# Kernel tuning notes

Hardware: AMD Instinct MI355X
Metric: run time of the kernel (lower is better)

The kernel has to match this reference:

```python
import jax, jax.numpy as jnp
import numpy as np
from jax import lax

PART = 224   # PART_IMAGE_SIZE
PAD = 224    # PAD_SIZE
TOPN = 4
IOU_THRESH = 0.25
N_ANCHORS = 1614


def _conv(x, w, b, stride, pad):
    y = lax.conv_general_dilated(x, w, (stride, stride), [(pad, pad), (pad, pad)],
                                 dimension_numbers=('NCHW', 'OIHW', 'NCHW'))
    return y + b[None, :, None, None]


def _iou(box, boxes):
    # box [4], boxes [N,4] as (y0,x0,y1,x1)
    yy0 = jnp.maximum(box[0], boxes[:, 0]); xx0 = jnp.maximum(box[1], boxes[:, 1])
    yy1 = jnp.minimum(box[2], boxes[:, 2]); xx1 = jnp.minimum(box[3], boxes[:, 3])
    inter = jnp.clip(yy1 - yy0, 0.0) * jnp.clip(xx1 - xx0, 0.0)
    a = (box[2] - box[0]) * (box[3] - box[1])
    areas = (boxes[:, 2] - boxes[:, 0]) * (boxes[:, 3] - boxes[:, 1])
    return inter / (a + areas - inter)


def _nms(scores, boxes):
    # hard NMS keeping TOPN boxes; returns indices [TOPN]
    valid = jnp.ones(scores.shape, dtype=bool)
    idxs = []
    for _ in range(TOPN):
        i = jnp.argmax(jnp.where(valid, scores, -jnp.inf))
        idxs.append(i)
        valid = valid & (_iou(boxes[i], boxes) <= IOU_THRESH)
    return jnp.stack(idxs)


def _crop_resize(img, box):
    # img [3,Hp,Wp] padded image, box [4] float; bilinear, align_corners=True,
    # matching F.interpolate(x_pad[:, :, y0:y1, x0:x1], (PART, PART))
    Hp, Wp = img.shape[1], img.shape[2]
    def coords(c0, c1, L):
        t = jnp.arange(PART, dtype=img.dtype) / (PART - 1)
        c = c0 + (c1 - 1.0 - c0) * t          # absolute source coordinate
        cf = jnp.floor(c)
        lo = jnp.clip(cf.astype(jnp.int32), 0, L - 1)
        hi = jnp.clip(lo + 1, 0, L - 1)
        return lo, hi, c - cf
    yl, yh, wy = coords(box[0], box[2], Hp)
    xl, xh, wx = coords(box[1], box[3], Wp)
    g = lambda yi, xi: img[:, yi[:, None], xi[None, :]]   # [3,PART,PART]
    return ((1 - wy)[:, None] * ((1 - wx) * g(yl, xl) + wx * g(yl, xh))
            + wy[:, None] * ((1 - wx) * g(yh, xl) + wx * g(yh, xh)))


def setup_inputs() -> dict:
    key = jax.random.key(0)
    ks = jax.random.split(key, 20)
    x = jax.random.uniform(ks[0], (16, 3, 448, 448), dtype=jnp.float32)
    rpn_feature = jax.random.normal(ks[1], (16, 2048, 14, 14), dtype=jnp.float32)
    # valid boxes inside the padded 896x896 image
    y0 = jax.random.randint(ks[2], (N_ANCHORS,), 0, 560)
    x0 = jax.random.randint(ks[3], (N_ANCHORS,), 0, 560)
    h = jax.random.randint(ks[4], (N_ANCHORS,), 32, 336)
    w = jax.random.randint(ks[5], (N_ANCHORS,), 32, 336)
    anchors = jnp.stack([y0, x0, jnp.minimum(y0 + h, 896), jnp.minimum(x0 + w, 896)], axis=1).astype(jnp.int32)
    s = 0.02
    inp = {
        'x': x, 'rpn_feature': rpn_feature, 'anchors': anchors,
        'w_down1': jax.random.normal(ks[6], (128, 2048, 3, 3), jnp.float32) * s,
        'b_down1': jnp.zeros((128,), jnp.float32),
        'w_down2': jax.random.normal(ks[7], (128, 128, 3, 3), jnp.float32) * s,
        'b_down2': jnp.zeros((128,), jnp.float32),
        'w_down3': jax.random.normal(ks[8], (128, 128, 3, 3), jnp.float32) * s,
        'b_down3': jnp.zeros((128,), jnp.float32),
        'w_tidy1': jax.random.normal(ks[9], (6, 128, 1, 1), jnp.float32) * s,
        'b_tidy1': jnp.zeros((6,), jnp.float32),
        'w_tidy2': jax.random.normal(ks[10], (6, 128, 1, 1), jnp.float32) * s,
        'b_tidy2': jnp.zeros((6,), jnp.float32),
        'w_tidy3': jax.random.normal(ks[11], (9, 128, 1, 1), jnp.float32) * s,
        'b_tidy3': jnp.zeros((9,), jnp.float32),
    }
    return inp


def reference(x, rpn_feature, anchors,
              w_down1, b_down1, w_down2, b_down2, w_down3, b_down3,
              w_tidy1, b_tidy1, w_tidy2, b_tidy2, w_tidy3, b_tidy3):
    B = x.shape[0]
    # ProposalNet
    d1 = jax.nn.relu(_conv(rpn_feature, w_down1, b_down1, 1, 1))   # [B,128,14,14]
    d2 = jax.nn.relu(_conv(d1, w_down2, b_down2, 2, 1))            # [B,128,7,7]
    d3 = jax.nn.relu(_conv(d2, w_down3, b_down3, 2, 1))            # [B,128,4,4]
    t1 = _conv(d1, w_tidy1, b_tidy1, 1, 0).reshape(B, -1)
    t2 = _conv(d2, w_tidy2, b_tidy2, 1, 0).reshape(B, -1)
    t3 = _conv(d3, w_tidy3, b_tidy3, 1, 0).reshape(B, -1)
    rpn_score = jnp.concatenate([t1, t2, t3], axis=1)              # [B, 1614]
    boxes = anchors.astype(x.dtype)                                # [N,4]
    top_n_index = jax.vmap(lambda s: _nms(s, boxes))(rpn_score)    # [B,TOPN]
    top_n_prob = jnp.take_along_axis(rpn_score, top_n_index, axis=1)
    x_pad = jnp.pad(x, ((0, 0), (0, 0), (PAD, PAD), (PAD, PAD)))   # [B,3,896,896]
    sel_boxes = boxes[top_n_index]                                 # [B,TOPN,4]
    part_imgs = jax.vmap(lambda img, bxs: jax.vmap(lambda b: _crop_resize(img, b))(bxs))(x_pad, sel_boxes)
    # part_imgs: [B,TOPN,3,PART,PART]
    return rpn_score, top_n_index, top_n_prob, part_imgs
```

## Files before the change

### kernel.cpp

```cpp
#include <hip/hip_runtime.h>
#include <hip/hip_bf16.h>

#define NB 16
#define NA 1614
#define NBP (NB * 196 * 128)

typedef __bf16 bf16x8 __attribute__((ext_vector_type(8)));
typedef float f32x4 __attribute__((ext_vector_type(4)));

__device__ __forceinline__ unsigned short f2bf(float v) {
  unsigned u = __float_as_uint(v);
  unsigned r = (u + 0x7FFFu + ((u >> 16) & 1u)) >> 16;
  return (unsigned short)r;
}
__device__ __forceinline__ float bf2f(unsigned short s) {
  return __uint_as_float(((unsigned)s) << 16);
}

__global__ __launch_bounds__(256)
void prep(const float* __restrict__ w, const float* __restrict__ in,
          unsigned short* __restrict__ wTh, unsigned short* __restrict__ wTl,
          unsigned short* __restrict__ aTh, unsigned short* __restrict__ aTl) {
  __shared__ float s[32 * 201];
  const int bid = blockIdx.x;
  if (bid < 1024) {
    const int chunk = bid & 63, b = bid >> 6;
    const float* src = in + ((size_t)b * 2048 + chunk * 32) * 196;
#pragma unroll
    for (int r = 0; r < 7; r++) {
      int e = threadIdx.x + 256 * r;
      if (e < 1568) {
        int ic = e / 49, f = e - ic * 49;
        float4 v = ((const float4*)(src + (size_t)ic * 196))[f];
        float* d = s + ic * 201 + f * 4;
        d[0] = v.x; d[1] = v.y; d[2] = v.z; d[3] = v.w;
      }
    }
    __syncthreads();
    unsigned short* oh = aTh + (size_t)bid * (196 * 32);
    unsigned short* ol = aTl + (size_t)bid * (196 * 32);
#pragma unroll
    for (int r = 0; r < 4; r++) {
      int e = threadIdx.x + 256 * r;
      if (e < 784) {
        int pos = e >> 2, part = e & 3;
        unsigned short hv[8], lv[8];
#pragma unroll
        for (int j = 0; j < 8; j++) {
          float v = s[(part * 8 + j) * 201 + pos];
          unsigned short h = f2bf(v);
          hv[j] = h;
          lv[j] = f2bf(v - bf2f(h));
        }
        ((uint4*)oh)[e] = *(uint4*)hv;
        ((uint4*)ol)[e] = *(uint4*)lv;
      }
    }
  } else {
    int e = (bid - 1024) * 256 + threadIdx.x;
    if (e < 9 * 128 * 2048) {
      int tap = e / (128 * 2048);
      int rem = e - tap * (128 * 2048);
      int oc = rem >> 11, ic = rem & 2047;
      int kcp = ic >> 7, ks = (ic >> 5) & 3, icq = (ic >> 3) & 3, j = ic & 7;
      size_t g2 = ((size_t)(kcp * 36 + tap * 4 + ks) << 12) + oc * 32 + icq * 8 + j;
      float v = w[((size_t)oc * 2048 + ic) * 9 + tap];
      unsigned short h = f2bf(v);
      wTh[g2] = h;
      wTl[g2] = f2bf(v - bf2f(h));
    }
  }
}

#define APL 2192
#define ABUF (4 * APL)

#define LOADB(H, L, T, K)                                                     \
  {                                                                           \
    const size_t o_ = ((size_t)(kc * 36 + (T) * 4 + (K)) << 12) + bln;        \
    const unsigned short* ph_ = wTh + o_;                                     \
    const unsigned short* pq_ = wTl + o_;                                     \
    H[0] = *(const bf16x8*)(ph_);                                             \
    H[1] = *(const bf16x8*)(ph_ + 512);                                       \
    H[2] = *(const bf16x8*)(ph_ + 1024);                                      \
    H[3] = *(const bf16x8*)(ph_ + 1536);                                      \
    L[0] = *(const bf16x8*)(pq_);                                             \
    L[1] = *(const bf16x8*)(pq_ + 512);                                       \
    L[2] = *(const bf16x8*)(pq_ + 1024);                                      \
    L[3] = *(const bf16x8*)(pq_ + 1536);                                      \
  }

#define STEP(IT, BUH, BUL, BNH, BNL)                                          \
  {                                                                           \
    const int it_ = (IT);                                                     \
    const int ks_ = it_ / 9, tap_ = it_ - ks_ * 9;                            \
    {             \
      const int ni_ = (it_ < 35) ? it_ + 1 : 35;                              \
      const int nk_ = ni_ / 9, nt_ = ni_ - nk_ * 9;                           \
      LOADB(BNH, BNL, nt_, nk_);                                              \
    }                                                                         \
    if (ks_ < 3) {   \
      const uint4* gh_ = (const uint4*)(aTh + ((size_t)(b * 64 + kc * 4 + ks_ + 1) * 196) * 32); \
      const uint4* gl_ = (const uint4*)(aTl + ((size_t)(b * 64 + kc * 4 + ks_ + 1) * 196) * 32); \
      if (tap_ >= 3 && tap_ <= 6) {                                           \
        int e_ = tid + 256 * (tap_ - 3);                                      \
        if (e_ < 784) {                                                       \
          int pos_ = e_ >> 2, part_ = e_ & 3;                                 \
          int py_ = pos_ / 14, px_ = pos_ - py_ * 14;                         \
          int d_ = (((ks_ + 1) & 1) ? ABUF : 0) + part_ * APL + (py_ + 1) * 136 + (px_ + 1) * 8; \
          *(uint4*)(sAh + d_) = sgh;                                          \
          *(uint4*)(sAl + d_) = sgl;                                          \
        }                                                                     \
      }                                                                       \
      if (tap_ >= 2 && tap_ <= 5) {                                           \
        int e_ = tid + 256 * (tap_ - 2);                                      \
        if (e_ < 784) { sgh = gh_[e_]; sgl = gl_[e_]; }                       \
      }                                                                       \
    }                                                                         \
    const int t8_ = (tap_ / 3) * 136 + (tap_ - (tap_ / 3) * 3) * 8;           \
    const unsigned short* pah_ = sAh + (ks_ & 1) * ABUF + qoff + t8_;         \
    const unsigned short* pal_ = sAl + (ks_ & 1) * ABUF + qoff + t8_;         \
    bf16x8 afh[7], afl[7];                                                    \
    _Pragma("unroll") for (int mf = 0; mf < 7; mf++) {                        \
      afh[mf] = *(const bf16x8*)(pah_ + abase[mf]);                           \
      afl[mf] = *(const bf16x8*)(pal_ + abase[mf]);                           \
    }                                                                         \
    _Pragma("unroll") for (int mf = 0; mf < 7; mf++)                          \
      _Pragma("unroll") for (int nf = 0; nf < 4; nf++)                        \
        acc[mf][nf] = __builtin_amdgcn_mfma_f32_16x16x32_bf16(afh[mf], BUH[nf], acc[mf][nf], 0, 0, 0); \
    _Pragma("unroll") for (int mf = 0; mf < 7; mf++)                          \
      _Pragma("unroll") for (int nf = 0; nf < 4; nf++)                        \
        acc[mf][nf] = __builtin_amdgcn_mfma_f32_16x16x32_bf16(afl[mf], BUH[nf], acc[mf][nf], 0, 0, 0); \
    _Pragma("unroll") for (int mf = 0; mf < 7; mf++)                          \
      _Pragma("unroll") for (int nf = 0; nf < 4; nf++)                        \
        acc[mf][nf] = __builtin_amdgcn_mfma_f32_16x16x32_bf16(afh[mf], BUL[nf], acc[mf][nf], 0, 0, 0); \
    if (tap_ == 8) __syncthreads();                                           \
  }

__global__ __launch_bounds__(256, 1)
void conv1_mfma(const unsigned short* __restrict__ aTh, const unsigned short* __restrict__ aTl,
                const unsigned short* __restrict__ wTh, const unsigned short* __restrict__ wTl,
                float* __restrict__ p1) {
  const int bid = blockIdx.x;
  const int kc = bid & 15;
  const int b  = bid >> 4;
  const int tid = threadIdx.x;
  const int wid = tid >> 6, lane = tid & 63;
  const int wm = wid & 1, wn = wid >> 1;
  const int q = lane >> 4, ln = lane & 15;

  __shared__ unsigned short sAh[2 * ABUF];
  __shared__ unsigned short sAl[2 * ABUF];

  for (int e = tid; e < ABUF; e += 256) {
    ((unsigned int*)sAh)[e] = 0u;
    ((unsigned int*)sAl)[e] = 0u;
  }

  int abase[7];
#pragma unroll
  for (int mf = 0; mf < 7; mf++) {
    int row = wm * 112 + mf * 16 + ln;
    int y = row / 14, x = row - y * 14;
    abase[mf] = (row < 196) ? (y * 136 + x * 8) : 0;
  }
  const int qoff = q * APL;
  const int bln = (wn * 64 + ln) * 32 + q * 8;

  f32x4 acc[7][4];
#pragma unroll
  for (int mf = 0; mf < 7; mf++)
#pragma unroll
    for (int nf = 0; nf < 4; nf++) acc[mf][nf] = (f32x4){0.f, 0.f, 0.f, 0.f};

  uint4 sgh, sgl;

  {
    const uint4* gh = (const uint4*)(aTh + ((size_t)(b * 64 + kc * 4) * 196) * 32);
    const uint4* gl = (const uint4*)(aTl + ((size_t)(b * 64 + kc * 4) * 196) * 32);
#pragma unroll
    for (int r = 0; r < 4; r++) {
      int e = tid + 256 * r;
      if (e < 784) {
        int pos = e >> 2, part = e & 3;
        int py = pos / 14, px = pos - py * 14;
        int d = part * APL + (py + 1) * 136 + (px + 1) * 8;
        *(uint4*)(sAh + d) = gh[e];
        *(uint4*)(sAl + d) = gl[e];
      }
    }
  }
  bf16x8 b0h[4], b0l[4], b1h[4], b1l[4];
  LOADB(b0h, b0l, 0, 0);
  __syncthreads();

  for (int it = 0; it < 36; it += 2) {
    STEP(it,     b0h, b0l, b1h, b1l);
    STEP(it + 1, b1h, b1l, b0h, b0l);
  }

  float* pk = p1 + ((size_t)kc * NB + b) * 196 * 128;
#pragma unroll
  for (int mf = 0; mf < 7; mf++) {
    const int row0 = wm * 112 + mf * 16 + q * 4;
#pragma unroll
    for (int nf = 0; nf < 4; nf++) {
      const int oc = wn * 64 + nf * 16 + ln;
#pragma unroll
      for (int r = 0; r < 4; r++) {
        const int row = row0 + r;
        if (row < 196) pk[(size_t)row * 128 + oc] = acc[mf][nf][r];
      }
    }
  }
}

__global__ __launch_bounds__(256)
void conv1_finish_p(const float* __restrict__ p1, const float* __restrict__ bias,
                    float* __restrict__ d1) {
  __shared__ float s[28 * 132];
  const int bid = blockIdx.x;
  const int pt = bid % 7, b = bid / 7;
  const int tid = threadIdx.x;
#pragma unroll
  for (int r = 0; r < 4; r++) {
    int u = tid + 256 * r;
    if (u < 896) {
      int pos = u >> 5, oc4 = u & 31;
      const float* base = p1 + ((size_t)(b * 196 + pt * 28 + pos)) * 128 + oc4 * 4;
      float4 sum = ((const float4*)bias)[oc4];
#pragma unroll
      for (int k = 0; k < 16; k++) {
        float4 v = *(const float4*)(base + (size_t)k * NBP);
        sum.x += v.x; sum.y += v.y; sum.z += v.z; sum.w += v.w;
      }
      sum.x = fmaxf(sum.x, 0.f); sum.y = fmaxf(sum.y, 0.f);
      sum.z = fmaxf(sum.z, 0.f); sum.w = fmaxf(sum.w, 0.f);
      *(float4*)(s + pos * 132 + oc4 * 4) = sum;
    }
  }
  __syncthreads();
#pragma unroll
  for (int r = 0; r < 4; r++) {
    int u = tid + 256 * r;
    if (u < 896) {
      int oc = u / 7, f = u - oc * 7;
      float4 v;
      v.x = s[(f * 4 + 0) * 132 + oc];
      v.y = s[(f * 4 + 1) * 132 + oc];
      v.z = s[(f * 4 + 2) * 132 + oc];
      v.w = s[(f * 4 + 3) * 132 + oc];
      *(float4*)(d1 + ((size_t)b * 128 + oc) * 196 + pt * 28 + f * 4) = v;
    }
  }
}

__global__ void conv2_part(const float* __restrict__ d1, const float* __restrict__ w,
                           float* __restrict__ p2) {
  const int bid = blockIdx.x;
  const int kc = bid & 3, oct = (bid >> 2) & 3, b = bid >> 4;
  const int ic0 = kc * 32, oc0 = oct * 32;
  const int tid = threadIdx.x;
  const int ocl = tid >> 3, rw = tid & 7;

  __shared__ float s_in[32 * 320];
  __shared__ float s_w[32 * 324];

#pragma unroll
  for (int r = 0; r < 32; r++) {
    const int e = tid + 256 * r;
    const int ch = e >> 8, idx = e & 255;
    const int tr = idx >> 4, tc = idx & 15;
    const int iy = tr - 1, ix = tc - 1;
    float v = 0.f;
    if ((unsigned)iy < 14u && (unsigned)ix < 14u)
      v = d1[((size_t)b * 128 + ic0 + ch) * 196 + iy * 14 + ix];
    s_in[ch * 320 + tr * 20 + tc] = v;
  }
#pragma unroll
  for (int r = 0; r < 36; r++) {
    const int e = tid + 256 * r;
    const int oc = e / 288, rem = e - oc * 288;
    const int ch = rem / 9, tap = rem - ch * 9;
    s_w[ch * 324 + tap * 36 + oc] =
        w[(size_t)(oc0 + oc) * 1152 + (size_t)ic0 * 9 + rem];
  }
  __syncthreads();

  if (rw < 7) {
    float acc[7] = {};
    for (int ic = 0; ic < 32; ic++) {
      const float* wrow = s_w + ic * 324 + ocl;
      const float* irow = s_in + ic * 320;
#pragma unroll
      for (int ky = 0; ky < 3; ky++) {
        const float* r = irow + (2 * rw + ky) * 20;
        const float4 f0 = *(const float4*)(r);
        const float4 f1 = *(const float4*)(r + 4);
        const float4 f2 = *(const float4*)(r + 8);
        const float4 f3 = *(const float4*)(r + 12);
        const float ev[8] = {f0.x, f0.z, f1.x, f1.z, f2.x, f2.z, f3.x, f3.z};
        const float od[7] = {f0.y, f0.w, f1.y, f1.w, f2.y, f2.w, f3.y};
        const float w0 = wrow[(ky * 3 + 0) * 36];
        const float w1 = wrow[(ky * 3 + 1) * 36];
        const float w2 = wrow[(ky * 3 + 2) * 36];
#pragma unroll
        for (int x = 0; x < 7; x++)
          acc[x] = fmaf(w0, ev[x], fmaf(w1, od[x], fmaf(w2, ev[x + 1], acc[x])));
      }
    }
    float* po = p2 + (((size_t)kc * NB + b) * 128 + oc0 + ocl) * 49 + rw * 7;
#pragma unroll
    for (int x = 0; x < 7; x++) po[x] = acc[x];
  }
}

__global__ void conv2_finish(const float* __restrict__ p2, const float* __restrict__ bias,
                             float* __restrict__ d2) {
  const int i = blockIdx.x * 256 + threadIdx.x;
  if (i >= NB * 128 * 49) return;
  const int oc = (i / 49) & 127;
  float s = bias[oc];
#pragma unroll
  for (int k = 0; k < 4; k++) s += p2[(size_t)k * (NB * 128 * 49) + i];
  d2[i] = fmaxf(s, 0.f);
}

__global__ void conv3_part(const float* __restrict__ d2, const float* __restrict__ w,
                           float* __restrict__ p3) {
  const int bid = blockIdx.x;
  const int kc = bid & 1, oct = (bid >> 1) & 7, b = bid >> 4;
  const int ic0 = kc * 64, oc0 = oct * 16;
  const int tid = threadIdx.x;
  const int oc = tid >> 4, p = tid & 15;
  const int y = p >> 2, x = p & 3;

  __shared__ float s_in[64 * 108];
  __shared__ float s_w[64 * 144];

#pragma unroll
  for (int r = 0; r < 21; r++) {
    const int e = tid + 256 * r;
    if (e < 64 * 81) {
      const int ch = e / 81, idx = e - ch * 81;
      const int tr = idx / 9, tc = idx - tr * 9;
      const int iy = tr - 1, ix = tc - 1;
      float v = 0.f;
      if ((unsigned)iy < 7u && (unsigned)ix < 7u)
        v = d2[((size_t)b * 128 + ic0 + ch) * 49 + iy * 7 + ix];
      s_in[ch * 108 + tr * 12 + tc] = v;
    }
  }
#pragma unroll
  for (int r = 0; r < 36; r++) {
    const int e = tid + 256 * r;
    const int o = e / 576, rem = e - o * 576;
    const int ch = rem / 9, tap = rem - ch * 9;
    s_w[ch * 144 + tap * 16 + o] =
        w[(size_t)(oc0 + o) * 1152 + (size_t)ic0 * 9 + rem];
  }
  __syncthreads();

  float acc = 0.f;
  for (int ic = 0; ic < 64; ic++) {
    const float* wrow = s_w + ic * 144 + oc;
    const float* irow = s_in + ic * 108 + 2 * y * 12 + 2 * x;
#pragma unroll
    for (int ky = 0; ky < 3; ky++)
#pragma unroll
      for (int kx = 0; kx < 3; kx++)
        acc = fmaf(wrow[(ky * 3 + kx) * 16], irow[ky * 12 + kx], acc);
  }
  p3[(((size_t)kc * NB + b) * 128 + oc0 + oc) * 16 + p] = acc;
}

__global__ __launch_bounds__(256, 1)
void score_nms(const float* __restrict__ d1, const float* __restrict__ d2,
               const float* __restrict__ p3, const float* __restrict__ bd3,
               const float* __restrict__ w1, const float* __restrict__ b1,
               const float* __restrict__ w2, const float* __restrict__ b2,
               const float* __restrict__ w3, const float* __restrict__ b3,
               const int* __restrict__ anchors, float* __restrict__ score,
               float* __restrict__ out_idx, float* __restrict__ out_prob,
               float* __restrict__ sel) {
  __shared__ float s_in[32 * 200];
  __shared__ float s_w[21 * 128];
  __shared__ float s_b[21];
  __shared__ float s_sc[NA];
  __shared__ float s_bx[NA * 4];
  __shared__ float r_s[256];
  __shared__ int r_i[256];
  const int b = blockIdx.x, tid = threadIdx.x;

  for (int i = tid; i < 768; i += 256) s_w[i] = w1[i];
  for (int i = tid; i < 768; i += 256) s_w[768 + i] = w2[i];
  for (int i = tid; i < 1152; i += 256) s_w[1536 + i] = w3[i];
  if (tid < 21) s_b[tid] = (tid < 6) ? b1[tid] : (tid < 12) ? b2[tid - 6] : b3[tid - 12];
  for (int i = tid; i < NA; i += 256) {
    s_bx[i * 4 + 0] = (float)anchors[i * 4 + 0];
    s_bx[i * 4 + 1] = (float)anchors[i * 4 + 1];
    s_bx[i * 4 + 2] = (float)anchors[i * 4 + 2];
    s_bx[i * 4 + 3] = (float)anchors[i * 4 + 3];
  }

  float acc[5] = {0.f, 0.f, 0.f, 0.f, 0.f};
  for (int chunk = 0; chunk < 4; chunk++) {
    __syncthreads();
    const float* src = d1 + ((size_t)b * 128 + chunk * 32) * 196;
#pragma unroll
    for (int r = 0; r < 7; r++) {
      int e = tid + 256 * r;
      if (e < 1568) {
        int ic = e / 49, f = e - ic * 49;
        *(float4*)(s_in + ic * 200 + f * 4) = ((const float4*)(src + (size_t)ic * 196))[f];
      }
    }
    __syncthreads();
#pragma unroll
    for (int k = 0; k < 5; k++) {
      int j = tid + 256 * k;
      if (j < 1176) {
        int oc = j / 196, p = j - oc * 196;
        const float* wr = s_w + oc * 128 + chunk * 32;
        float s = acc[k];
#pragma unroll
        for (int ic = 0; ic < 32; ic++) s = fmaf(wr[ic], s_in[ic * 200 + p], s);
        acc[k] = s;
      }
    }
  }
#pragma unroll
  for (int k = 0; k < 5; k++) {
    int j = tid + 256 * k;
    if (j < 1176) {
      int oc = j / 196;
      float s = acc[k] + s_b[oc];
      s_sc[j] = s;
      score[b * NA + j] = s;
    }
  }

  __syncthreads();
  {
    const float* src = d2 + (size_t)b * 6272;
#pragma unroll
    for (int r = 0; r < 7; r++) {
      int e = tid + 256 * r;
      if (e < 1568) *(float4*)(s_in + e * 4) = ((const float4*)src)[e];
    }
  }
  __syncthreads();
#pragma unroll
  for (int k = 0; k < 2; k++) {
    int jj = tid + 256 * k;
    if (jj < 294) {
      int oc = jj / 49, p = jj - oc * 49;
      const float* wr = s_w + 768 + oc * 128;
      float s = s_b[6 + oc];
#pragma unroll 8
      for (int ic = 0; ic < 128; ic++) s = fmaf(wr[ic], s_in[ic * 49 + p], s);
      s_sc[1176 + jj] = s;
      score[b * NA + 1176 + jj] = s;
    }
  }

  __syncthreads();
  {
    const float4* s0 = (const float4*)(p3 + (size_t)b * 2048);
    const float4* s1 = (const float4*)(p3 + 32768 + (size_t)b * 2048);
#pragma unroll
    for (int r = 0; r < 2; r++) {
      int e = tid + 256 * r;
      if (e < 512) {
        float4 a = s0[e], c = s1[e];
        float bb = bd3[e >> 2];
        float4 v;
        v.x = fmaxf(a.x + c.x + bb, 0.f);
        v.y = fmaxf(a.y + c.y + bb, 0.f);
        v.z = fmaxf(a.z + c.z + bb, 0.f);
        v.w = fmaxf(a.w + c.w + bb, 0.f);
        *(float4*)(s_in + e * 4) = v;
      }
    }
  }
  __syncthreads();
  if (tid < 144) {
    int oc = tid >> 4, p = tid & 15;
    const float* wr = s_w + 1536 + oc * 128;
    float s = s_b[12 + oc];
#pragma unroll 8
    for (int ic = 0; ic < 128; ic++) s = fmaf(wr[ic], s_in[ic * 16 + p], s);
    s_sc[1470 + tid] = s;
    score[b * NA + 1470 + tid] = s;
  }
  __syncthreads();

  for (int t = 0; t < 4; t++) {
    float bs = -__builtin_inff();
    int bi = NA;
    for (int i = tid; i < NA; i += 256) {
      float s = s_sc[i];
      if (s > bs || (s == bs && i < bi)) { bs = s; bi = i; }
    }
    r_s[tid] = bs; r_i[tid] = bi;
    __syncthreads();
    for (int off = 128; off > 0; off >>= 1) {
      if (tid < off) {
        float s2 = r_s[tid + off]; int i2 = r_i[tid + off];
        if (s2 > r_s[tid] || (s2 == r_s[tid] && i2 < r_i[tid])) { r_s[tid] = s2; r_i[tid] = i2; }
      }
      __syncthreads();
    }
    const int idx = r_i[0];
    const float by0 = s_bx[idx * 4 + 0], bx0 = s_bx[idx * 4 + 1];
    const float by1 = s_bx[idx * 4 + 2], bx1 = s_bx[idx * 4 + 3];
    if (tid == 0) {
      out_idx[b * 4 + t] = (float)idx;
      out_prob[b * 4 + t] = s_sc[idx];
      sel[(b * 4 + t) * 4 + 0] = by0;
      sel[(b * 4 + t) * 4 + 1] = bx0;
      sel[(b * 4 + t) * 4 + 2] = by1;
      sel[(b * 4 + t) * 4 + 3] = bx1;
    }
    __syncthreads();
    const float a = (by1 - by0) * (bx1 - bx0);
    for (int i = tid; i < NA; i += 256) {
      float cy0 = s_bx[i * 4 + 0], cx0 = s_bx[i * 4 + 1];
      float cy1 = s_bx[i * 4 + 2], cx1 = s_bx[i * 4 + 3];
      float yy0 = fmaxf(by0, cy0), xx0 = fmaxf(bx0, cx0);
      float yy1 = fminf(by1, cy1), xx1 = fminf(bx1, cx1);
      float inter = fmaxf(yy1 - yy0, 0.f) * fmaxf(xx1 - xx0, 0.f);
      float ar = (cy1 - cy0) * (cx1 - cx0);
      float iou = inter / (a + ar - inter);
      if (iou > 0.25f) s_sc[i] = -__builtin_inff();
    }
    __syncthreads();
  }
}

__global__ void crop_kernel(const float* __restrict__ x, const float* __restrict__ sel,
                            float* __restrict__ out) {
  int i4 = blockIdx.x * 256 + threadIdx.x;
  const int total4 = NB * 4 * 3 * 224 * 56;
  if (i4 >= total4) return;
  int px0 = (i4 % 56) * 4;
  int t = i4 / 56;
  int py = t % 224; t /= 224;
  int ch = t % 3;  t /= 3;
  int n  = t % 4;
  int b  = t / 4;

  const float* bx = sel + (b * 4 + n) * 4;
  const float y0 = bx[0], x0 = bx[1], y1 = bx[2], x1 = bx[3];

  float ty = (float)py / 223.0f;
  float cy = y0 + (y1 - 1.0f - y0) * ty;
  float cyf = floorf(cy);
  int ylo = (int)cyf; ylo = ylo < 0 ? 0 : (ylo > 895 ? 895 : ylo);
  int yhi = ylo + 1 > 895 ? 895 : ylo + 1;
  float wy = cy - cyf;

  const float* img = x + ((size_t)b * 3 + ch) * 448 * 448;
  auto g = [&](int yy, int xx) -> float {
    yy -= 224; xx -= 224;
    if ((unsigned)yy < 448u && (unsigned)xx < 448u)
      return img[(size_t)yy * 448 + xx];
    return 0.f;
  };

  float4 res;
  float* rp = &res.x;
#pragma unroll
  for (int k = 0; k < 4; k++) {
    float tx = (float)(px0 + k) / 223.0f;
    float cx = x0 + (x1 - 1.0f - x0) * tx;
    float cxf = floorf(cx);
    int xlo = (int)cxf; xlo = xlo < 0 ? 0 : (xlo > 895 ? 895 : xlo);
    int xhi = xlo + 1 > 895 ? 895 : xlo + 1;
    float wx = cx - cxf;
    float v00 = g(ylo, xlo), v01 = g(ylo, xhi);
    float v10 = g(yhi, xlo), v11 = g(yhi, xhi);
    rp[k] = (1.f - wy) * ((1.f - wx) * v00 + wx * v01) +
            wy * ((1.f - wx) * v10 + wx * v11);
  }
  *(float4*)(out + (size_t)i4 * 4) = res;
}

extern "C" void kernel_launch(void* const* d_in, const int* in_sizes, int n_in,
                              void* d_out, int out_size, void* d_ws, size_t ws_size,
                              hipStream_t stream) {
  const float* x    = (const float*)d_in[0];
  const float* rpn  = (const float*)d_in[1];
  const int*   anc  = (const int*)d_in[2];
  const float* w_d1 = (const float*)d_in[3];
  const float* b_d1 = (const float*)d_in[4];
  const float* w_d2 = (const float*)d_in[5];
  const float* b_d2 = (const float*)d_in[6];
  const float* w_d3 = (const float*)d_in[7];
  const float* b_d3 = (const float*)d_in[8];
  const float* w_t1 = (const float*)d_in[9];
  const float* b_t1 = (const float*)d_in[10];
  const float* w_t2 = (const float*)d_in[11];
  const float* b_t2 = (const float*)d_in[12];
  const float* w_t3 = (const float*)d_in[13];
  const float* b_t3 = (const float*)d_in[14];

  float* out = (float*)d_out;
  float* ws = (float*)d_ws;

  float* d1  = ws;
  float* d2  = d1 + 401408;
  float* d3  = d2 + 100352;
  float* sel = d3 + 32768;
  float* p2  = sel + 256;
  float* p3  = p2 + 401408;
  unsigned short* wTh = (unsigned short*)(p3 + 65536);
  unsigned short* wTl = wTh + 2359296;
  unsigned short* aTh = wTl + 2359296;
  unsigned short* aTl = aTh + 6422528;

  float* score    = out;
  float* out_idx  = out + 25824;
  float* out_prob = out + 25888;
  float* parts    = out + 25952;
  float* p1       = parts;

  prep<<<dim3(10240), dim3(256), 0, stream>>>(w_d1, rpn, wTh, wTl, aTh, aTl);
  conv1_mfma<<<dim3(256), dim3(256), 0, stream>>>(aTh, aTl, wTh, wTl, p1);
  conv1_finish_p<<<dim3(112), dim3(256), 0, stream>>>(p1, b_d1, d1);
  conv2_part<<<dim3(256), dim3(256), 0, stream>>>(d1, w_d2, p2);
  conv2_finish<<<dim3(392), dim3(256), 0, stream>>>(p2, b_d2, d2);
  conv3_part<<<dim3(256), dim3(256), 0, stream>>>(d2, w_d3, p3);
  score_nms<<<dim3(16), dim3(256), 0, stream>>>(d1, d2, p3, b_d3, w_t1, b_t1, w_t2, b_t2,
                                                w_t3, b_t3, anc, score, out_idx, out_prob, sel);
  crop_kernel<<<dim3(9408), dim3(256), 0, stream>>>(x, sel, parts);
}
```

Baseline: 274.6 us.

## Split conv1 K-loop across two warp groups with shared-memory reduction

Doubles the conv1_mfma block to 512 threads. Two groups of four waves each handle half of the four K sub-chunks, using separate double-buffered LDS activation tiles. The second group writes its partial accumulators to LDS and the first group adds them before writing p1. This shortens the serial K loop per wave and adds latency hiding, at the cost of more LDS, an extra reduction pass and higher register pressure under the new launch bounds.

```diff
diff --git a/kernel.cpp b/kernel.cpp
--- a/kernel.cpp
+++ b/kernel.cpp
@@ -92,34 +92,34 @@
 
 #define STEP(IT, BUH, BUL, BNH, BNL)                                          \
   {                                                                           \
-    const int it_ = (IT);                                                     \
-    const int ks_ = it_ / 9, tap_ = it_ - ks_ * 9;                            \
+    const int it_ = (IT);                               \
+    const int lks_ = it_ / 9, tap_ = it_ - lks_ * 9;                          \
     {             \
-      const int ni_ = (it_ < 35) ? it_ + 1 : 35;                              \
-      const int nk_ = ni_ / 9, nt_ = ni_ - nk_ * 9;                           \
-      LOADB(BNH, BNL, nt_, nk_);                                              \
+      const int ni_ = (it_ < 17) ? it_ + 1 : 17;                              \
+      const int nlk_ = ni_ / 9, nt_ = ni_ - nlk_ * 9;                         \
+      LOADB(BNH, BNL, nt_, wk * 2 + nlk_);                                    \
     }                                                                         \
-    if (ks_ < 3) {   \
-      const uint4* gh_ = (const uint4*)(aTh + ((size_t)(b * 64 + kc * 4 + ks_ + 1) * 196) * 32); \
-      const uint4* gl_ = (const uint4*)(aTl + ((size_t)(b * 64 + kc * 4 + ks_ + 1) * 196) * 32); \
+    if (lks_ == 0) {  \
+      const uint4* gh_ = (const uint4*)(aTh + ((size_t)(b * 64 + kc * 4 + wk * 2 + 1) * 196) * 32); \
+      const uint4* gl_ = (const uint4*)(aTl + ((size_t)(b * 64 + kc * 4 + wk * 2 + 1) * 196) * 32); \
       if (tap_ >= 3 && tap_ <= 6) {                                           \
-        int e_ = tid + 256 * (tap_ - 3);                                      \
+        int e_ = htid + 256 * (tap_ - 3);                                     \
         if (e_ < 784) {                                                       \
           int pos_ = e_ >> 2, part_ = e_ & 3;                                 \
           int py_ = pos_ / 14, px_ = pos_ - py_ * 14;                         \
-          int d_ = (((ks_ + 1) & 1) ? ABUF : 0) + part_ * APL + (py_ + 1) * 136 + (px_ + 1) * 8; \
+          int d_ = abufbase + ABUF + part_ * APL + (py_ + 1) * 136 + (px_ + 1) * 8; \
           *(uint4*)(sAh + d_) = sgh;                                          \
           *(uint4*)(sAl + d_) = sgl;                                          \
         }                                                                     \
       }                                                                       \
       if (tap_ >= 2 && tap_ <= 5) {                                           \
-        int e_ = tid + 256 * (tap_ - 2);                                      \
+        int e_ = htid + 256 * (tap_ - 2);                                     \
         if (e_ < 784) { sgh = gh_[e_]; sgl = gl_[e_]; }                       \
       }                                                                       \
     }                                                                         \
     const int t8_ = (tap_ / 3) * 136 + (tap_ - (tap_ / 3) * 3) * 8;           \
-    const unsigned short* pah_ = sAh + (ks_ & 1) * ABUF + qoff + t8_;         \
-    const unsigned short* pal_ = sAl + (ks_ & 1) * ABUF + qoff + t8_;         \
+    const unsigned short* pah_ = sAh + abufbase + (lks_ & 1) * ABUF + qoff + t8_; \
+    const unsigned short* pal_ = sAl + abufbase + (lks_ & 1) * ABUF + qoff + t8_; \
     bf16x8 afh[7], afl[7];                                                    \
     _Pragma("unroll") for (int mf = 0; mf < 7; mf++) {                        \
       afh[mf] = *(const bf16x8*)(pah_ + abase[mf]);                           \
@@ -137,7 +137,7 @@
     if (tap_ == 8) __syncthreads();                                           \
   }
 
-__global__ __launch_bounds__(256, 1)
+__global__ __launch_bounds__(512, 2)
 void conv1_mfma(const unsigned short* __restrict__ aTh, const unsigned short* __restrict__ aTl,
                 const unsigned short* __restrict__ wTh, const unsigned short* __restrict__ wTl,
                 float* __restrict__ p1) {
@@ -145,14 +145,17 @@
   const int kc = bid & 15;
   const int b  = bid >> 4;
   const int tid = threadIdx.x;
+  const int htid = tid & 255;
   const int wid = tid >> 6, lane = tid & 63;
-  const int wm = wid & 1, wn = wid >> 1;
+  const int wq = wid & 3, wk = wid >> 2;
+  const int wm = wq & 1, wn = wq >> 1;
   const int q = lane >> 4, ln = lane & 15;
 
-  __shared__ unsigned short sAh[2 * ABUF];
-  __shared__ unsigned short sAl[2 * ABUF];
-
-  for (int e = tid; e < ABUF; e += 256) {
+  __shared__ unsigned short sAh[4 * ABUF];
+  __shared__ unsigned short sAl[4 * ABUF];
+  const int abufbase = wk * (2 * ABUF);
+
+  for (int e = tid; e < 2 * ABUF; e += 512) {
     ((unsigned int*)sAh)[e] = 0u;
     ((unsigned int*)sAl)[e] = 0u;
   }
@@ -175,41 +178,64 @@
 
   uint4 sgh, sgl;
 
+  __syncthreads();
+
   {
-    const uint4* gh = (const uint4*)(aTh + ((size_t)(b * 64 + kc * 4) * 196) * 32);
-    const uint4* gl = (const uint4*)(aTl + ((size_t)(b * 64 + kc * 4) * 196) * 32);
+    const uint4* gh = (const uint4*)(aTh + ((size_t)(b * 64 + kc * 4 + wk * 2) * 196) * 32);
+    const uint4* gl = (const uint4*)(aTl + ((size_t)(b * 64 + kc * 4 + wk * 2) * 196) * 32);
 #pragma unroll
     for (int r = 0; r < 4; r++) {
-      int e = tid + 256 * r;
+      int e = htid + 256 * r;
       if (e < 784) {
         int pos = e >> 2, part = e & 3;
         int py = pos / 14, px = pos - py * 14;
-        int d = part * APL + (py + 1) * 136 + (px + 1) * 8;
+        int d = abufbase + part * APL + (py + 1) * 136 + (px + 1) * 8;
         *(uint4*)(sAh + d) = gh[e];
         *(uint4*)(sAl + d) = gl[e];
       }
     }
   }
   bf16x8 b0h[4], b0l[4], b1h[4], b1l[4];
-  LOADB(b0h, b0l, 0, 0);
-  __syncthreads();
-
-  for (int it = 0; it < 36; it += 2) {
+  LOADB(b0h, b0l, 0, wk * 2);
+  __syncthreads();
+
+  for (int it = 0; it < 18; it += 2) {
     STEP(it,     b0h, b0l, b1h, b1l);
     STEP(it + 1, b1h, b1l, b0h, b0l);
   }
 
-  float* pk = p1 + ((size_t)kc * NB + b) * 196 * 128;
-#pragma unroll
-  for (int mf = 0; mf < 7; mf++) {
-    const int row0 = wm * 112 + mf * 16 + q * 4;
-#pragma unroll
-    for (int nf = 0; nf < 4; nf++) {
-      const int oc = wn * 64 + nf * 16 + ln;
-#pragma unroll
-      for (int r = 0; r < 4; r++) {
-        const int row = row0 + r;
-        if (row < 196) pk[(size_t)row * 128 + oc] = acc[mf][nf][r];
+  if (wk == 1) {
+    float* rb = (wq < 2 ? (float*)sAh : (float*)sAl) + (wq & 1) * 7168;
+#pragma unroll
+    for (int mf = 0; mf < 7; mf++)
+#pragma unroll
+      for (int nf = 0; nf < 4; nf++)
+        *(f32x4*)(rb + (mf * 4 + nf) * 256 + lane * 4) = acc[mf][nf];
+  }
+  __syncthreads();
+  if (wk == 0) {
+    const float* rb = (wq < 2 ? (const float*)sAh : (const float*)sAl) + (wq & 1) * 7168;
+#pragma unroll
+    for (int mf = 0; mf < 7; mf++)
+#pragma unroll
+      for (int nf = 0; nf < 4; nf++) {
+        f32x4 v = *(const f32x4*)(rb + (mf * 4 + nf) * 256 + lane * 4);
+        acc[mf][nf][0] += v[0]; acc[mf][nf][1] += v[1];
+        acc[mf][nf][2] += v[2]; acc[mf][nf][3] += v[3];
+      }
+
+    float* pk = p1 + ((size_t)kc * NB + b) * 196 * 128;
+#pragma unroll
+    for (int mf = 0; mf < 7; mf++) {
+      const int row0 = wm * 112 + mf * 16 + q * 4;
+#pragma unroll
+      for (int nf = 0; nf < 4; nf++) {
+        const int oc = wn * 64 + nf * 16 + ln;
+#pragma unroll
+        for (int r = 0; r < 4; r++) {
+          const int row = row0 + r;
+          if (row < 196) pk[(size_t)row * 128 + oc] = acc[mf][nf][r];
+        }
       }
     }
   }
@@ -626,7 +652,7 @@
   float* p1       = parts;
 
   prep<<<dim3(10240), dim3(256), 0, stream>>>(w_d1, rpn, wTh, wTl, aTh, aTl);
-  conv1_mfma<<<dim3(256), dim3(256), 0, stream>>>(aTh, aTl, wTh, wTl, p1);
+  conv1_mfma<<<dim3(256), dim3(512), 0, stream>>>(aTh, aTl, wTh, wTl, p1);
   conv1_finish_p<<<dim3(112), dim3(256), 0, stream>>>(p1, b_d1, d1);
   conv2_part<<<dim3(256), dim3(256), 0, stream>>>(d1, w_d2, p2);
   conv2_finish<<<dim3(392), dim3(256), 0, stream>>>(p2, b_d2, d2);
```

Measured after the change: 282.0 us. 2.7% more time.

## Split conv1 MFMA blocks by output-row half to double grid and occupancy

Applied to the files above, without the earlier changes.

The conv1 implicit-GEMM kernel now launches 512 blocks instead of 256, each covering half the spatial rows (with a halo) and all 128 output channels split across four waves. Each block stages only the activation rows it needs into a smaller shared buffer, and per-thread accumulator and B-fragment registers are halved so that two blocks can share a CU. The aim is better occupancy and latency hiding on a grid that previously filled only 256 CUs. In exchange, weight fragments and the halo rows are loaded twice, once by each half.

```diff
diff --git a/kernel.cpp b/kernel.cpp
--- a/kernel.cpp
+++ b/kernel.cpp
@@ -72,7 +72,7 @@
   }
 }
 
-#define APL 2192
+#define APL 1360
 #define ABUF (4 * APL)
 
 #define LOADB(H, L, T, K)                                                     \
@@ -82,12 +82,8 @@
     const unsigned short* pq_ = wTl + o_;                                     \
     H[0] = *(const bf16x8*)(ph_);                                             \
     H[1] = *(const bf16x8*)(ph_ + 512);                                       \
-    H[2] = *(const bf16x8*)(ph_ + 1024);                                      \
-    H[3] = *(const bf16x8*)(ph_ + 1536);                                      \
     L[0] = *(const bf16x8*)(pq_);                                             \
     L[1] = *(const bf16x8*)(pq_ + 512);                                       \
-    L[2] = *(const bf16x8*)(pq_ + 1024);                                      \
-    L[3] = *(const bf16x8*)(pq_ + 1536);                                      \
   }
 
 #define STEP(IT, BUH, BUL, BNH, BNL)                                          \
@@ -99,22 +95,24 @@
       const int nk_ = ni_ / 9, nt_ = ni_ - nk_ * 9;                           \
       LOADB(BNH, BNL, nt_, nk_);                                              \
     }                                                                         \
-    if (ks_ < 3) {   \
-      const uint4* gh_ = (const uint4*)(aTh + ((size_t)(b * 64 + kc * 4 + ks_ + 1) * 196) * 32); \
-      const uint4* gl_ = (const uint4*)(aTl + ((size_t)(b * 64 + kc * 4 + ks_ + 1) * 196) * 32); \
-      if (tap_ >= 3 && tap_ <= 6) {                                           \
+    if (ks_ < 3) {        \
+      if (tap_ == 3 || tap_ == 4) {                                           \
         int e_ = tid + 256 * (tap_ - 3);                                      \
-        if (e_ < 784) {                                                       \
-          int pos_ = e_ >> 2, part_ = e_ & 3;                                 \
+        if (e_ < ne) {                                                        \
+          int u_ = pos04 + e_;                                                \
+          int pos_ = u_ >> 2, part_ = u_ & 3;                                 \
           int py_ = pos_ / 14, px_ = pos_ - py_ * 14;                         \
-          int d_ = (((ks_ + 1) & 1) ? ABUF : 0) + part_ * APL + (py_ + 1) * 136 + (px_ + 1) * 8; \
+          int d_ = (((ks_ + 1) & 1) ? ABUF : 0) + part_ * APL                 \
+                   + (py_ + 1 - rowoff) * 136 + (px_ + 1) * 8;                \
           *(uint4*)(sAh + d_) = sgh;                                          \
           *(uint4*)(sAl + d_) = sgl;                                          \
         }                                                                     \
       }                                                                       \
-      if (tap_ >= 2 && tap_ <= 5) {                                           \
+      if (tap_ == 2 || tap_ == 3) {                                           \
+        const uint4* gh_ = (const uint4*)(aTh + ((size_t)(b * 64 + kc * 4 + ks_ + 1) * 196) * 32); \
+        const uint4* gl_ = (const uint4*)(aTl + ((size_t)(b * 64 + kc * 4 + ks_ + 1) * 196) * 32); \
         int e_ = tid + 256 * (tap_ - 2);                                      \
-        if (e_ < 784) { sgh = gh_[e_]; sgl = gl_[e_]; }                       \
+        if (e_ < ne) { sgh = gh_[pos04 + e_]; sgl = gl_[pos04 + e_]; }        \
       }                                                                       \
     }                                                                         \
     const int t8_ = (tap_ / 3) * 136 + (tap_ - (tap_ / 3) * 3) * 8;           \
@@ -126,33 +124,39 @@
       afl[mf] = *(const bf16x8*)(pal_ + abase[mf]);                           \
     }                                                                         \
     _Pragma("unroll") for (int mf = 0; mf < 7; mf++)                          \
-      _Pragma("unroll") for (int nf = 0; nf < 4; nf++)                        \
+      _Pragma("unroll") for (int nf = 0; nf < 2; nf++)                        \
         acc[mf][nf] = __builtin_amdgcn_mfma_f32_16x16x32_bf16(afh[mf], BUH[nf], acc[mf][nf], 0, 0, 0); \
     _Pragma("unroll") for (int mf = 0; mf < 7; mf++)                          \
-      _Pragma("unroll") for (int nf = 0; nf < 4; nf++)                        \
+      _Pragma("unroll") for (int nf = 0; nf < 2; nf++)                        \
         acc[mf][nf] = __builtin_amdgcn_mfma_f32_16x16x32_bf16(afl[mf], BUH[nf], acc[mf][nf], 0, 0, 0); \
     _Pragma("unroll") for (int mf = 0; mf < 7; mf++)                          \
-      _Pragma("unroll") for (int nf = 0; nf < 4; nf++)                        \
+      _Pragma("unroll") for (int nf = 0; nf < 2; nf++)                        \
         acc[mf][nf] = __builtin_amdgcn_mfma_f32_16x16x32_bf16(afh[mf], BUL[nf], acc[mf][nf], 0, 0, 0); \
     if (tap_ == 8) __syncthreads();                                           \
   }
 
-__global__ __launch_bounds__(256, 1)
+__global__ __launch_bounds__(256, 2)
 void conv1_mfma(const unsigned short* __restrict__ aTh, const unsigned short* __restrict__ aTl,
                 const unsigned short* __restrict__ wTh, const unsigned short* __restrict__ wTl,
                 float* __restrict__ p1) {
   const int bid = blockIdx.x;
   const int kc = bid & 15;
-  const int b  = bid >> 4;
+  const int b  = (bid >> 4) & 15;
+  const int mh = bid >> 8;
   const int tid = threadIdx.x;
   const int wid = tid >> 6, lane = tid & 63;
-  const int wm = wid & 1, wn = wid >> 1;
+  const int wn = wid;
   const int q = lane >> 4, ln = lane & 15;
 
   __shared__ unsigned short sAh[2 * ABUF];
   __shared__ unsigned short sAl[2 * ABUF];
 
-  for (int e = tid; e < ABUF; e += 256) {
+  const int rowoff = 6 * mh;
+  const int pos0 = mh ? 98 : 0;
+  const int ne   = mh ? 392 : 504;
+  const int pos04 = pos0 * 4;
+
+  for (int e = tid; e < 2 * ABUF / 2; e += 256) {
     ((unsigned int*)sAh)[e] = 0u;
     ((unsigned int*)sAl)[e] = 0u;
   }
@@ -160,37 +164,40 @@
   int abase[7];
 #pragma unroll
   for (int mf = 0; mf < 7; mf++) {
-    int row = wm * 112 + mf * 16 + ln;
+    int row = mh * 112 + mf * 16 + ln;
     int y = row / 14, x = row - y * 14;
-    abase[mf] = (row < 196) ? (y * 136 + x * 8) : 0;
+    abase[mf] = (row < 196) ? ((y - rowoff) * 136 + x * 8) : 0;
   }
   const int qoff = q * APL;
-  const int bln = (wn * 64 + ln) * 32 + q * 8;
-
-  f32x4 acc[7][4];
+  const int bln = (wn * 32 + ln) * 32 + q * 8;
+
+  f32x4 acc[7][2];
 #pragma unroll
   for (int mf = 0; mf < 7; mf++)
 #pragma unroll
-    for (int nf = 0; nf < 4; nf++) acc[mf][nf] = (f32x4){0.f, 0.f, 0.f, 0.f};
-
-  uint4 sgh, sgl;
+    for (int nf = 0; nf < 2; nf++) acc[mf][nf] = (f32x4){0.f, 0.f, 0.f, 0.f};
+
+  uint4 sgh = {}, sgl = {};
+
+  __syncthreads();
 
   {
     const uint4* gh = (const uint4*)(aTh + ((size_t)(b * 64 + kc * 4) * 196) * 32);
     const uint4* gl = (const uint4*)(aTl + ((size_t)(b * 64 + kc * 4) * 196) * 32);
 #pragma unroll
-    for (int r = 0; r < 4; r++) {
+    for (int r = 0; r < 2; r++) {
       int e = tid + 256 * r;
-      if (e < 784) {
-        int pos = e >> 2, part = e & 3;
+      if (e < ne) {
+        int u = pos04 + e;
+        int pos = u >> 2, part = u & 3;
         int py = pos / 14, px = pos - py * 14;
-        int d = part * APL + (py + 1) * 136 + (px + 1) * 8;
-        *(uint4*)(sAh + d) = gh[e];
-        *(uint4*)(sAl + d) = gl[e];
-      }
-    }
-  }
-  bf16x8 b0h[4], b0l[4], b1h[4], b1l[4];
+        int d = part * APL + (py + 1 - rowoff) * 136 + (px + 1) * 8;
+        *(uint4*)(sAh + d) = gh[u];
+        *(uint4*)(sAl + d) = gl[u];
+      }
+    }
+  }
+  bf16x8 b0h[2], b0l[2], b1h[2], b1l[2];
   LOADB(b0h, b0l, 0, 0);
   __syncthreads();
 
@@ -202,10 +209,10 @@
   float* pk = p1 + ((size_t)kc * NB + b) * 196 * 128;
 #pragma unroll
   for (int mf = 0; mf < 7; mf++) {
-    const int row0 = wm * 112 + mf * 16 + q * 4;
-#pragma unroll
-    for (int nf = 0; nf < 4; nf++) {
-      const int oc = wn * 64 + nf * 16 + ln;
+    const int row0 = mh * 112 + mf * 16 + q * 4;
+#pragma unroll
+    for (int nf = 0; nf < 2; nf++) {
+      const int oc = wn * 32 + nf * 16 + ln;
 #pragma unroll
       for (int r = 0; r < 4; r++) {
         const int row = row0 + r;
@@ -626,7 +633,7 @@
   float* p1       = parts;
 
   prep<<<dim3(10240), dim3(256), 0, stream>>>(w_d1, rpn, wTh, wTl, aTh, aTl);
-  conv1_mfma<<<dim3(256), dim3(256), 0, stream>>>(aTh, aTl, wTh, wTl, p1);
+  conv1_mfma<<<dim3(512), dim3(256), 0, stream>>>(aTh, aTl, wTh, wTl, p1);
   conv1_finish_p<<<dim3(112), dim3(256), 0, stream>>>(p1, b_d1, d1);
   conv2_part<<<dim3(256), dim3(256), 0, stream>>>(d1, w_d2, p2);
   conv2_finish<<<dim3(392), dim3(256), 0, stream>>>(p2, b_d2, d2);
```

After: 275.9 us. Within noise of the previous version (+0.5%).

## Coalesce weight transpose via LDS and read conv1 activations straight from global

Applied to the files above, without the earlier changes.

The weight-prep branch of prep now stages a 32-oc by 32-ic by 9-tap tile in shared memory with float4 loads, then writes the transposed bf16 hi/lo pairs. This replaces the strided per-element gather that took 9216 blocks, so the grid drops to 1280 blocks. Separately, conv1_mfma no longer double-buffers padded activation tiles in LDS. Each MFMA A-fragment is loaded directly from global (L2-cached) with bounds masking for the 3x3 halo, which removes LDS traffic and barriers but adds more global loads per step.

```diff
diff --git a/kernel.cpp b/kernel.cpp
--- a/kernel.cpp
+++ b/kernel.cpp
@@ -21,7 +21,7 @@
 void prep(const float* __restrict__ w, const float* __restrict__ in,
           unsigned short* __restrict__ wTh, unsigned short* __restrict__ wTl,
           unsigned short* __restrict__ aTh, unsigned short* __restrict__ aTl) {
-  __shared__ float s[32 * 201];
+  __shared__ float sbuf[32 * 289];
   const int bid = blockIdx.x;
   if (bid < 1024) {
     const int chunk = bid & 63, b = bid >> 6;
@@ -32,7 +32,7 @@
       if (e < 1568) {
         int ic = e / 49, f = e - ic * 49;
         float4 v = ((const float4*)(src + (size_t)ic * 196))[f];
-        float* d = s + ic * 201 + f * 4;
+        float* d = sbuf + ic * 201 + f * 4;
         d[0] = v.x; d[1] = v.y; d[2] = v.z; d[3] = v.w;
       }
     }
@@ -47,7 +47,7 @@
         unsigned short hv[8], lv[8];
 #pragma unroll
         for (int j = 0; j < 8; j++) {
-          float v = s[(part * 8 + j) * 201 + pos];
+          float v = sbuf[(part * 8 + j) * 201 + pos];
           unsigned short h = f2bf(v);
           hv[j] = h;
           lv[j] = f2bf(v - bf2f(h));
@@ -57,23 +57,32 @@
       }
     }
   } else {
-    int e = (bid - 1024) * 256 + threadIdx.x;
-    if (e < 9 * 128 * 2048) {
-      int tap = e / (128 * 2048);
-      int rem = e - tap * (128 * 2048);
-      int oc = rem >> 11, ic = rem & 2047;
-      int kcp = ic >> 7, ks = (ic >> 5) & 3, icq = (ic >> 3) & 3, j = ic & 7;
-      size_t g2 = ((size_t)(kcp * 36 + tap * 4 + ks) << 12) + oc * 32 + icq * 8 + j;
-      float v = w[((size_t)oc * 2048 + ic) * 9 + tap];
+    const int bid2 = bid - 1024;
+    const int ocg = bid2 & 3, ks = (bid2 >> 2) & 3, kcp = bid2 >> 4;
+    const int oc0 = ocg * 32;
+    const int ic0 = kcp * 128 + ks * 32;
+#pragma unroll
+    for (int r = 0; r < 9; r++) {
+      int f = threadIdx.x + 256 * r;
+      int o = f / 72, rem4 = f - o * 72;
+      float4 v = *(const float4*)(w + ((size_t)(oc0 + o) * 2048 + ic0) * 9 + rem4 * 4);
+      float* d = sbuf + o * 289 + rem4 * 4;
+      d[0] = v.x; d[1] = v.y; d[2] = v.z; d[3] = v.w;
+    }
+    __syncthreads();
+#pragma unroll
+    for (int r = 0; r < 36; r++) {
+      int e = threadIdx.x + 256 * r;
+      int tap = e >> 10, rem = e & 1023;
+      int o = rem >> 5, ic = rem & 31;
+      float v = sbuf[o * 289 + ic * 9 + tap];
       unsigned short h = f2bf(v);
+      size_t g2 = ((size_t)(kcp * 36 + tap * 4 + ks) << 12) + oc0 * 32 + rem;
       wTh[g2] = h;
       wTl[g2] = f2bf(v - bf2f(h));
     }
   }
 }
-
-#define APL 2192
-#define ABUF (4 * APL)
 
 #define LOADB(H, L, T, K)                                                     \
   {                                                                           \
@@ -94,36 +103,26 @@
   {                                                                           \
     const int it_ = (IT);                                                     \
     const int ks_ = it_ / 9, tap_ = it_ - ks_ * 9;                            \
+    const int dy_ = tap_ / 3 - 1;                                             \
+    const int dx_ = tap_ - (tap_ / 3) * 3 - 1;                                \
+    const int td_ = (ks_ * 196 + dy_ * 14 + dx_) * 4;        \
+    bf16x8 afh[7], afl[7];                                                    \
+    _Pragma("unroll") for (int mf = 0; mf < 7; mf++) {                        \
+      uint4 vh_ = gA0h[td_ + aoff[mf]];                                       \
+      uint4 vl_ = gA0l[td_ + aoff[mf]];                                       \
+      bool ok_ = ((unsigned)(ay[mf] + dy_) < 14u) &&                          \
+                 ((unsigned)(ax[mf] + dx_) < 14u);                            \
+      if (!ok_) {                                                             \
+        vh_.x = 0u; vh_.y = 0u; vh_.z = 0u; vh_.w = 0u;                       \
+        vl_.x = 0u; vl_.y = 0u; vl_.z = 0u; vl_.w = 0u;                       \
+      }                                                                       \
+      afh[mf] = *(const bf16x8*)&vh_;                                         \
+      afl[mf] = *(const bf16x8*)&vl_;                                         \
+    }                                                                         \
     {             \
       const int ni_ = (it_ < 35) ? it_ + 1 : 35;                              \
       const int nk_ = ni_ / 9, nt_ = ni_ - nk_ * 9;                           \
       LOADB(BNH, BNL, nt_, nk_);                                              \
-    }                                                                         \
-    if (ks_ < 3) {   \
-      const uint4* gh_ = (const uint4*)(aTh + ((size_t)(b * 64 + kc * 4 + ks_ + 1) * 196) * 32); \
-      const uint4* gl_ = (const uint4*)(aTl + ((size_t)(b * 64 + kc * 4 + ks_ + 1) * 196) * 32); \
-      if (tap_ >= 3 && tap_ <= 6) {                                           \
-        int e_ = tid + 256 * (tap_ - 3);                                      \
-        if (e_ < 784) {                                                       \
-          int pos_ = e_ >> 2, part_ = e_ & 3;                                 \
-          int py_ = pos_ / 14, px_ = pos_ - py_ * 14;                         \
-          int d_ = (((ks_ + 1) & 1) ? ABUF : 0) + part_ * APL + (py_ + 1) * 136 + (px_ + 1) * 8; \
-          *(uint4*)(sAh + d_) = sgh;                                          \
-          *(uint4*)(sAl + d_) = sgl;                                          \
-        }                                                                     \
-      }                                                                       \
-      if (tap_ >= 2 && tap_ <= 5) {                                           \
-        int e_ = tid + 256 * (tap_ - 2);                                      \
-        if (e_ < 784) { sgh = gh_[e_]; sgl = gl_[e_]; }                       \
-      }                                                                       \
-    }                                                                         \
-    const int t8_ = (tap_ / 3) * 136 + (tap_ - (tap_ / 3) * 3) * 8;           \
-    const unsigned short* pah_ = sAh + (ks_ & 1) * ABUF + qoff + t8_;         \
-    const unsigned short* pal_ = sAl + (ks_ & 1) * ABUF + qoff + t8_;         \
-    bf16x8 afh[7], afl[7];                                                    \
-    _Pragma("unroll") for (int mf = 0; mf < 7; mf++) {                        \
-      afh[mf] = *(const bf16x8*)(pah_ + abase[mf]);                           \
-      afl[mf] = *(const bf16x8*)(pal_ + abase[mf]);                           \
     }                                                                         \
     _Pragma("unroll") for (int mf = 0; mf < 7; mf++)                          \
       _Pragma("unroll") for (int nf = 0; nf < 4; nf++)                        \
@@ -134,7 +133,6 @@
     _Pragma("unroll") for (int mf = 0; mf < 7; mf++)                          \
       _Pragma("unroll") for (int nf = 0; nf < 4; nf++)                        \
         acc[mf][nf] = __builtin_amdgcn_mfma_f32_16x16x32_bf16(afh[mf], BUL[nf], acc[mf][nf], 0, 0, 0); \
-    if (tap_ == 8) __syncthreads();                                           \
   }
 
 __global__ __launch_bounds__(256, 1)
@@ -149,50 +147,30 @@
   const int wm = wid & 1, wn = wid >> 1;
   const int q = lane >> 4, ln = lane & 15;
 
-  __shared__ unsigned short sAh[2 * ABUF];
-  __shared__ unsigned short sAl[2 * ABUF];
-
-  for (int e = tid; e < ABUF; e += 256) {
-    ((unsigned int*)sAh)[e] = 0u;
-    ((unsigned int*)sAl)[e] = 0u;
-  }
-
-  int abase[7];
+  int ay[7], ax[7], aoff[7];
 #pragma unroll
   for (int mf = 0; mf < 7; mf++) {
     int row = wm * 112 + mf * 16 + ln;
-    int y = row / 14, x = row - y * 14;
-    abase[mf] = (row < 196) ? (y * 136 + x * 8) : 0;
-  }
-  const int qoff = q * APL;
+    int v = (row < 196);
+    int y = v ? row / 14 : 0;
+    int x = v ? (row - y * 14) : 0;
+    if (!v) y = 0;
+    ay[mf] = y; ax[mf] = x;
+    aoff[mf] = (y * 14 + x) * 4 + q;
+  }
   const int bln = (wn * 64 + ln) * 32 + q * 8;
 
+  const uint4* gA0h = (const uint4*)(aTh + (size_t)(b * 64 + kc * 4) * 6272);
+  const uint4* gA0l = (const uint4*)(aTl + (size_t)(b * 64 + kc * 4) * 6272);
+
   f32x4 acc[7][4];
 #pragma unroll
   for (int mf = 0; mf < 7; mf++)
 #pragma unroll
     for (int nf = 0; nf < 4; nf++) acc[mf][nf] = (f32x4){0.f, 0.f, 0.f, 0.f};
 
-  uint4 sgh, sgl;
-
-  {
-    const uint4* gh = (const uint4*)(aTh + ((size_t)(b * 64 + kc * 4) * 196) * 32);
-    const uint4* gl = (const uint4*)(aTl + ((size_t)(b * 64 + kc * 4) * 196) * 32);
-#pragma unroll
-    for (int r = 0; r < 4; r++) {
-      int e = tid + 256 * r;
-      if (e < 784) {
-        int pos = e >> 2, part = e & 3;
-        int py = pos / 14, px = pos - py * 14;
-        int d = part * APL + (py + 1) * 136 + (px + 1) * 8;
-        *(uint4*)(sAh + d) = gh[e];
-        *(uint4*)(sAl + d) = gl[e];
-      }
-    }
-  }
   bf16x8 b0h[4], b0l[4], b1h[4], b1l[4];
   LOADB(b0h, b0l, 0, 0);
-  __syncthreads();
 
   for (int it = 0; it < 36; it += 2) {
     STEP(it,     b0h, b0l, b1h, b1l);
@@ -625,7 +603,7 @@
   float* parts    = out + 25952;
   float* p1       = parts;
 
-  prep<<<dim3(10240), dim3(256), 0, stream>>>(w_d1, rpn, wTh, wTl, aTh, aTl);
+  prep<<<dim3(1280), dim3(256), 0, stream>>>(w_d1, rpn, wTh, wTl, aTh, aTl);
   conv1_mfma<<<dim3(256), dim3(256), 0, stream>>>(aTh, aTl, wTh, wTl, p1);
   conv1_finish_p<<<dim3(112), dim3(256), 0, stream>>>(p1, b_d1, d1);
   conv2_part<<<dim3(256), dim3(256), 0, stream>>>(d1, w_d2, p2);
```

Result: slower. 313.3 us (+14.1%).
